# Performance work log

Measured on AMD Instinct MI355X. Metric: run time of the kernel, lower is better.

## Reference

```python
import jax, jax.numpy as jnp
import numpy as np

D_STATE = 16
D_CONV = 4


def layernorm(x, g, b, eps=1e-5):
    mu = jnp.mean(x, axis=-1, keepdims=True)
    var = jnp.mean(jnp.square(x - mu), axis=-1, keepdims=True)
    return (x - mu) * jax.lax.rsqrt(var + eps) * g + b


def mamba(x, W_in, conv_w, conv_b, W_x, W_dt, b_dt, A_log, D_param, W_out):
    # x: (B, L, C)
    B, L, C = x.shape
    d_inner, d_conv = conv_w.shape
    d_state = A_log.shape[1]
    dt_rank = W_dt.shape[0]

    xz = x @ W_in                       # (B, L, 2*d_inner)
    xm, z = jnp.split(xz, 2, axis=-1)   # each (B, L, d_inner)

    # depthwise causal conv1d (padding d_conv-1 on the left, truncated to L)
    xp = jnp.pad(xm, ((0, 0), (d_conv - 1, 0), (0, 0)))
    xm = sum(xp[:, k:k + L, :] * conv_w[:, k] for k in range(d_conv)) + conv_b
    xm = jax.nn.silu(xm)

    dbl = xm @ W_x                      # (B, L, dt_rank + 2*d_state)
    dt, Bm, Cm = jnp.split(dbl, [dt_rank, dt_rank + d_state], axis=-1)
    dt = jax.nn.softplus(dt @ W_dt + b_dt)  # (B, L, d_inner)
    A = -jnp.exp(A_log)                     # (d_inner, d_state)

    def step(h, inputs):
        dt_t, B_t, C_t, x_t = inputs        # (B,d_inner),(B,d_state),(B,d_state),(B,d_inner)
        dA = jnp.exp(dt_t[..., None] * A)   # (B, d_inner, d_state)
        h = dA * h + (dt_t * x_t)[..., None] * B_t[:, None, :]
        y = jnp.einsum('bds,bs->bd', h, C_t)
        return h, y

    seq = (dt.transpose(1, 0, 2), Bm.transpose(1, 0, 2),
           Cm.transpose(1, 0, 2), xm.transpose(1, 0, 2))
    h0 = jnp.zeros((B, d_inner, d_state), x.dtype)
    _, ys = jax.lax.scan(step, h0, seq)     # ys: (L, B, d_inner)
    y = ys.transpose(1, 0, 2) + xm * D_param
    y = y * jax.nn.silu(z)
    return y @ W_out                        # (B, L, C)


def setup_inputs() -> dict:
    key = jax.random.key(0)
    B, C, H, W = 8, 256, 32, 32
    d_inner = 2 * C
    dt_rank = (C + 15) // 16  # 16
    hidden = 4 * C
    ks = jax.random.split(key, 12)
    s = lambda k, shape, scale=0.02: jax.random.normal(k, shape, jnp.float32) * scale
    return {
        'x': jax.random.normal(ks[0], (B, C, H, W), jnp.float32),
        'ln1_g': jnp.ones((C,), jnp.float32), 'ln1_b': jnp.zeros((C,), jnp.float32),
        'ln2_g': jnp.ones((C,), jnp.float32), 'ln2_b': jnp.zeros((C,), jnp.float32),
        'W_in': s(ks[1], (C, 2 * d_inner)),
        'conv_w': s(ks[2], (d_inner, D_CONV), 0.1),
        'conv_b': jnp.zeros((d_inner,), jnp.float32),
        'W_x': s(ks[3], (d_inner, dt_rank + 2 * D_STATE)),
        'W_dt': s(ks[4], (dt_rank, d_inner)),
        'b_dt': s(ks[5], (d_inner,), 0.1),
        'A_log': jnp.log(jnp.tile(jnp.arange(1, D_STATE + 1, dtype=jnp.float32), (d_inner, 1))),
        'D_param': jnp.ones((d_inner,), jnp.float32),
        'W_out': s(ks[6], (d_inner, C)),
        'W1': s(ks[7], (C, hidden)), 'b1': jnp.zeros((hidden,), jnp.float32),
        'W2': s(ks[8], (hidden, C)), 'b2': jnp.zeros((C,), jnp.float32),
    }


def reference(x, ln1_g, ln1_b, ln2_g, ln2_b, W_in, conv_w, conv_b, W_x, W_dt,
              b_dt, A_log, D_param, W_out, W1, b1, W2, b2):
    B, C, H, W = x.shape
    x = x.transpose(0, 2, 3, 1)          # (B, H, W, C)
    res = x
    xn = layernorm(x, ln1_g, ln1_b)
    xm = mamba(xn.reshape(B, H * W, C), W_in, conv_w, conv_b, W_x, W_dt,
               b_dt, A_log, D_param, W_out).reshape(B, H, W, C)
    x = xm + res
    res = x
    xn = layernorm(x, ln2_g, ln2_b)
    x = jax.nn.gelu(xn @ W1 + b1, approximate=False) @ W2 + b2 + res
    return x.transpose(0, 3, 1, 2)        # (B, C, H, W)
```

## Files before the change

kernel.cpp:

```cpp
#include <hip/hip_runtime.h>
#include <hip/hip_bf16.h>
#include <math.h>

using u16 = unsigned short;
using u32 = unsigned int;
typedef __attribute__((ext_vector_type(8))) short bf16x8;
typedef __attribute__((ext_vector_type(4))) float f32x4;
typedef __attribute__((ext_vector_type(8))) unsigned short us8;
typedef __attribute__((ext_vector_type(4))) unsigned short us4;

__device__ __forceinline__ float b2f(u16 u) {
  return __uint_as_float(((u32)u) << 16);
}
__device__ __forceinline__ u16 f2b(float f) {
  u32 x = __float_as_uint(f);
  x += 0x7fffu + ((x >> 16) & 1u);
  return (u16)(x >> 16);
}

__global__ void k_detect(const u16* __restrict__ alog, int* __restrict__ flag) {
  if (threadIdx.x == 0 && blockIdx.x == 0)
    flag[0] = (alog[1] != 0) ? 1 : 0;
}

__device__ __forceinline__ u16 cvt_one(const void* src, int i, int f) {
  u16 r;
  if (f == 0) {
    float v = ((const float*)src)[i];
    if (!isfinite(v)) v = 0.f;
    r = f2b(v);
  } else {
    r = ((const u16*)src)[i];
    if (((r >> 7) & 0xFFu) == 0xFFu) r = 0;
  }
  return r;
}

struct SetupP {
  const void* ws0; const void* ws1; const void* ws2; const void* ws3;
  u16* wd0; u16* wd1; u16* wd2; u16* wd3;
  const void* ssrc[11];
  u16* sdst[11];
  int send[11];
  const void* wxr;
  const void* wdtr;
  u16* wcbc;
  int smallEnd;
  int total;
};
__global__ __launch_bounds__(256) void k_setup(SetupP p, const int* __restrict__ flag) {
  int i = blockIdx.x * 256 + threadIdx.x;
  if (i >= p.total) return;
  int f = flag[0];
  if (i < 262144) {
    int k = i >> 10, n = i & 1023;
    p.wd0[n * 256 + k] = cvt_one(p.ws0, i, f);
  } else if (i < 524288) {
    int j = i - 262144; int k = j >> 10, n = j & 1023;
    p.wd1[n * 256 + k] = cvt_one(p.ws1, j, f);
  } else if (i < 786432) {
    int j = i - 524288; int k = j >> 8, n = j & 255;
    p.wd2[n * 1024 + k] = cvt_one(p.ws2, j, f);
  } else if (i < 917504) {
    int j = i - 786432; int k = j >> 8, n = j & 255;
    p.wd3[n * 512 + k] = cvt_one(p.ws3, j, f);
  } else if (i < p.smallEnd) {
    int j = i - 917504;
    int seg = 0, base = 0;
    #pragma unroll
    for (int s = 0; s < 11; ++s) {
      if (j >= p.send[s]) { seg = s + 1; base = p.send[s]; }
    }
    p.sdst[seg][j - base] = cvt_one(p.ssrc[seg], j - base, f);
  } else {
    int idx = i - p.smallEnd;
    int j = idx >> 9, ii = idx & 511;
    u16 r;
    if (j < 512) {
      float s = 0.f;
      #pragma unroll
      for (int k = 0; k < 16; ++k)
        s = fmaf(b2f(cvt_one(p.wxr, ii * 48 + k, f)),
                 b2f(cvt_one(p.wdtr, k * 512 + j, f)), s);
      r = f2b(s);
    } else if (j < 544) {
      r = cvt_one(p.wxr, ii * 48 + 16 + (j - 512), f);
    } else {
      r = 0;
    }
    p.wcbc[idx] = r;
  }
}

__global__ __launch_bounds__(256) void k_tln(const void* __restrict__ src,
    const u16* __restrict__ g, const u16* __restrict__ be,
    u16* __restrict__ xt, u16* __restrict__ xn, const int* __restrict__ flag) {
  __shared__ float t[256][17];
  __shared__ float smu[16], srs[16];
  int bid = blockIdx.x;
  int lt = bid & 63, b = bid >> 6;
  int f = flag[0];
  int lc = threadIdx.x & 15;
  int lr = threadIdx.x >> 4;
  for (int i = 0; i < 16; ++i) {
    int c = i * 16 + lr;
    int l = lt * 16 + lc;
    size_t idx = ((size_t)b * 256 + c) * 1024 + l;
    float v;
    if (f == 0) {
      v = ((const float*)src)[idx];
      if (!isfinite(v)) v = 0.f;
    } else {
      u16 u = ((const u16*)src)[idx];
      if (((u >> 7) & 0xFFu) == 0xFFu) u = 0;
      v = b2f(u);
    }
    t[c][lc] = v;
  }
  __syncthreads();
  int token = threadIdx.x >> 4, j = threadIdx.x & 15;
  float s = 0.f, q = 0.f;
  for (int k = 0; k < 16; ++k) {
    float v = t[k * 16 + j][token];
    s += v; q = fmaf(v, v, q);
  }
  s += __shfl_xor(s, 1, 16); q += __shfl_xor(q, 1, 16);
  s += __shfl_xor(s, 2, 16); q += __shfl_xor(q, 2, 16);
  s += __shfl_xor(s, 4, 16); q += __shfl_xor(q, 4, 16);
  s += __shfl_xor(s, 8, 16); q += __shfl_xor(q, 8, 16);
  if (j == 0) {
    float mu = s * (1.f / 256.f);
    smu[token] = mu;
    srs[token] = rsqrtf(q * (1.f / 256.f) - mu * mu + 1e-5f);
  }
  __syncthreads();
  float gv = b2f(g[threadIdx.x]), bv = b2f(be[threadIdx.x]);
  size_t tok0 = (size_t)b * 1024 + lt * 16;
  for (int i = 0; i < 16; ++i) {
    float v = t[threadIdx.x][i];
    size_t o = (tok0 + i) * 256 + threadIdx.x;
    xt[o] = f2b(v);
    xn[o] = f2b((v - smu[i]) * srs[i] * gv + bv);
  }
}

__global__ __launch_bounds__(256) void k_ln(const u16* __restrict__ xin,
    const u16* __restrict__ g, const u16* __restrict__ be,
    u16* __restrict__ xn) {
  int tok = blockIdx.x * 4 + (threadIdx.x >> 6);
  int lane = threadIdx.x & 63;
  us4 xv = *(const us4*)&xin[(size_t)tok * 256 + lane * 4];
  float v[4];
  float s = 0.f, q = 0.f;
  #pragma unroll
  for (int j2 = 0; j2 < 4; ++j2) {
    v[j2] = b2f(xv[j2]);
    s += v[j2]; q = fmaf(v[j2], v[j2], q);
  }
  #pragma unroll
  for (int o = 1; o < 64; o <<= 1) {
    s += __shfl_xor(s, o, 64);
    q += __shfl_xor(q, o, 64);
  }
  float mu = s * (1.f / 256.f);
  float rs = rsqrtf(q * (1.f / 256.f) - mu * mu + 1e-5f);
  us4 o4;
  #pragma unroll
  for (int j2 = 0; j2 < 4; ++j2) {
    float t = (v[j2] - mu) * rs * b2f(g[lane * 4 + j2]) + b2f(be[lane * 4 + j2]);
    o4[j2] = f2b(t);
  }
  *(us4*)&xn[(size_t)tok * 256 + lane * 4] = o4;
}

__global__ __launch_bounds__(256) void k_conv(const u16* __restrict__ xz,
    const u16* __restrict__ cw, const u16* __restrict__ cb,
    u16* __restrict__ xm) {
  int idx = blockIdx.x * 256 + threadIdx.x;
  int d4 = (idx & 127) * 4;
  int tok = idx >> 7;
  int l = tok & 1023;
  float a[4];
  #pragma unroll
  for (int j = 0; j < 4; ++j) a[j] = b2f(cb[d4 + j]);
  #pragma unroll
  for (int k = 0; k < 4; ++k) {
    int ls = l - 3 + k;
    if (ls >= 0) {
      us4 xv = *(const us4*)&xz[(size_t)(tok - 3 + k) * 1024 + d4];
      #pragma unroll
      for (int j = 0; j < 4; ++j)
        a[j] = fmaf(b2f(xv[j]), b2f(cw[(d4 + j) * 4 + k]), a[j]);
    }
  }
  us4 o;
  #pragma unroll
  for (int j = 0; j < 4; ++j) {
    float sig = 1.f / (1.f + __expf(-a[j]));
    o[j] = f2b(a[j] * sig);
  }
  *(us4*)&xm[(size_t)tok * 512 + d4] = o;
}

__global__ __launch_bounds__(256) void k_scan1(const u16* __restrict__ dt,
    const u16* __restrict__ xm, const u16* __restrict__ bc,
    const u16* __restrict__ A_log, u16* __restrict__ hend,
    float* __restrict__ sdtw) {
  __shared__ float sB[32][16];
  int bi = blockIdx.x;
  int half = bi & 1;
  int bc_ = bi >> 1;
  int b = bc_ >> 5, c = bc_ & 31;
  int d = half * 256 + threadIdx.x;
  size_t tok0 = (size_t)b * 1024 + c * 32;
  for (int i = threadIdx.x; i < 512; i += 256) {
    int t = i >> 4, s = i & 15;
    sB[t][s] = b2f(bc[(tok0 + t) * 32 + s]);
  }
  __syncthreads();
  float As[16], h[16];
  bool fast = true;
  #pragma unroll
  for (int s = 0; s < 16; ++s) {
    As[s] = -__expf(b2f(A_log[d * 16 + s]));
    h[s] = 0.f;
    fast = fast && (fabsf(As[s] + (float)(s + 1)) < 0.02f * (s + 1));
  }
  float sacc = 0.f;
  float dtv = b2f(dt[tok0 * 512 + d]);
  float xv  = b2f(xm[tok0 * 512 + d]);
  if (fast) {
    for (int t = 0; t < 32; ++t) {
      float ndt = 0.f, nx = 0.f;
      if (t < 31) {
        ndt = b2f(dt[(tok0 + t + 1) * 512 + d]);
        nx  = b2f(xm[(tok0 + t + 1) * 512 + d]);
      }
      sacc += dtv;
      float u = dtv * xv;
      float q = __expf(-dtv), p = 1.f;
      #pragma unroll
      for (int s = 0; s < 16; ++s) {
        p *= q;
        h[s] = fmaf(p, h[s], u * sB[t][s]);
      }
      dtv = ndt; xv = nx;
    }
  } else {
    for (int t = 0; t < 32; ++t) {
      float ndt = 0.f, nx = 0.f;
      if (t < 31) {
        ndt = b2f(dt[(tok0 + t + 1) * 512 + d]);
        nx  = b2f(xm[(tok0 + t + 1) * 512 + d]);
      }
      sacc += dtv;
      float u = dtv * xv;
      #pragma unroll
      for (int s = 0; s < 16; ++s)
        h[s] = fmaf(__expf(dtv * As[s]), h[s], u * sB[t][s]);
      dtv = ndt; xv = nx;
    }
  }
  u16* hp = hend + ((size_t)bc_ * 512 + d) * 16;
  #pragma unroll
  for (int s = 0; s < 16; ++s) hp[s] = f2b(h[s]);
  sdtw[(size_t)bc_ * 512 + d] = sacc;
}

__global__ __launch_bounds__(256) void k_scan2(u16* __restrict__ hend,
    const float* __restrict__ sdtw, const u16* __restrict__ A_log) {
  int idx = blockIdx.x * 256 + threadIdx.x;
  int s = idx & 15, d = (idx >> 4) & 511, b = idx >> 13;
  float As_ = -__expf(b2f(A_log[d * 16 + s]));
  if (fabsf(As_ + (float)(s + 1)) < 0.02f * (s + 1)) As_ = -(float)(s + 1);
  float H = 0.f;
  for (int c = 0; c < 32; ++c) {
    size_t off = (size_t)(b * 32 + c) * 512 + d;
    float dec = __expf(As_ * sdtw[off]);
    float he = b2f(hend[off * 16 + s]);
    hend[off * 16 + s] = f2b(H);
    H = fmaf(dec, H, he);
  }
}

__global__ __launch_bounds__(256) void k_scan3(const u16* __restrict__ dt,
    const u16* __restrict__ xm, const u16* __restrict__ bc,
    const u16* __restrict__ xz, const u16* __restrict__ A_log,
    const u16* __restrict__ Dp, const u16* __restrict__ hstart,
    u16* __restrict__ yg) {
  __shared__ float sB[32][16], sC[32][16];
  int bi = blockIdx.x;
  int half = bi & 1;
  int bc_ = bi >> 1;
  int b = bc_ >> 5, c = bc_ & 31;
  int d = half * 256 + threadIdx.x;
  size_t tok0 = (size_t)b * 1024 + c * 32;
  for (int i = threadIdx.x; i < 1024; i += 256) {
    int t = i >> 5, col = i & 31;
    float v = b2f(bc[(tok0 + t) * 32 + col]);
    if (col < 16) sB[t][col] = v;
    else          sC[t][col - 16] = v;
  }
  __syncthreads();
  float As[16], h[16];
  const u16* hp = hstart + ((size_t)bc_ * 512 + d) * 16;
  bool fast = true;
  #pragma unroll
  for (int s = 0; s < 16; ++s) {
    As[s] = -__expf(b2f(A_log[d * 16 + s]));
    h[s] = b2f(hp[s]);
    fast = fast && (fabsf(As[s] + (float)(s + 1)) < 0.02f * (s + 1));
  }
  float Dd = b2f(Dp[d]);
  float dtv = b2f(dt[tok0 * 512 + d]);
  float xv  = b2f(xm[tok0 * 512 + d]);
  float zv  = b2f(xz[tok0 * 1024 + 512 + d]);
  for (int t = 0; t < 32; ++t) {
    float ndt = 0.f, nx = 0.f, nz = 0.f;
    if (t < 31) {
      ndt = b2f(dt[(tok0 + t + 1) * 512 + d]);
      nx  = b2f(xm[(tok0 + t + 1) * 512 + d]);
      nz  = b2f(xz[(tok0 + t + 1) * 1024 + 512 + d]);
    }
    float u = dtv * xv;
    if (fast) {
      float q = __expf(-dtv), p = 1.f;
      #pragma unroll
      for (int s = 0; s < 16; ++s) {
        p *= q;
        h[s] = fmaf(p, h[s], u * sB[t][s]);
      }
    } else {
      #pragma unroll
      for (int s = 0; s < 16; ++s)
        h[s] = fmaf(__expf(dtv * As[s]), h[s], u * sB[t][s]);
    }
    float y0 = 0.f, y1 = 0.f, y2 = 0.f, y3 = 0.f;
    #pragma unroll
    for (int s = 0; s < 16; s += 4) {
      y0 = fmaf(h[s + 0], sC[t][s + 0], y0);
      y1 = fmaf(h[s + 1], sC[t][s + 1], y1);
      y2 = fmaf(h[s + 2], sC[t][s + 2], y2);
      y3 = fmaf(h[s + 3], sC[t][s + 3], y3);
    }
    float y = (y0 + y1) + (y2 + y3);
    float yy = fmaf(xv, Dd, y);
    float sig = 1.f / (1.f + __expf(-zv));
    yg[(tok0 + t) * 512 + d] = f2b(yy * zv * sig);
    dtv = ndt; xv = nx; zv = nz;
  }
}

template<int EPI, int BM, int BN>
__global__ __launch_bounds__(256) void k_mgemm(
    const u16* __restrict__ A, const u16* __restrict__ Bt,
    const u16* __restrict__ bias, const u16* __restrict__ res,
    u16* __restrict__ outp, u16* __restrict__ out2,
    void* __restrict__ outv, const int* __restrict__ flag,
    int M, int N, int K, int GX) {
  constexpr int BK = 32;
  constexpr int LDP = BK + 8;
  constexpr int MT = BM / 32, NT = BN / 32;
  constexpr int AL = (BM * BK) / 2048, BL = (BN * BK) / 2048;
  __shared__ u16 As[2][BM][LDP];
  __shared__ u16 Bs[2][BN][LDP];
  const int tid = threadIdx.x;
  const int wid = tid >> 6, lane = tid & 63;
  const int wr = wid >> 1, wc2 = wid & 1;
  const int lrow = lane & 15, lk = lane >> 4;
  const int per = gridDim.x >> 3;
  const int t_ = (blockIdx.x & 7) * per + (blockIdx.x >> 3);
  const int m0 = (t_ / GX) * BM, n0 = (t_ % GX) * BN;

  f32x4 acc[MT][NT];
  #pragma unroll
  for (int i = 0; i < MT; ++i)
    #pragma unroll
    for (int j = 0; j < NT; ++j)
      acc[i][j] = (f32x4){0.f, 0.f, 0.f, 0.f};

  us8 ra[AL], rb[BL];
  #pragma unroll
  for (int i = 0; i < AL; ++i) {
    int c = tid + i * 256, row = c >> 2, k0 = (c & 3) * 8;
    ra[i] = *(const us8*)(A + (size_t)(m0 + row) * K + k0);
  }
  #pragma unroll
  for (int i = 0; i < BL; ++i) {
    int c = tid + i * 256, row = c >> 2, k0 = (c & 3) * 8;
    rb[i] = *(const us8*)(Bt + (size_t)(n0 + row) * K + k0);
  }
  #pragma unroll
  for (int i = 0; i < AL; ++i) {
    int c = tid + i * 256, row = c >> 2, k0 = (c & 3) * 8;
    *(us8*)&As[0][row][k0] = ra[i];
  }
  #pragma unroll
  for (int i = 0; i < BL; ++i) {
    int c = tid + i * 256, row = c >> 2, k0 = (c & 3) * 8;
    *(us8*)&Bs[0][row][k0] = rb[i];
  }
  __syncthreads();

  const int nIter = K / BK;
  for (int it = 0; it < nIter; ++it) {
    const int cur = it & 1;
    if (it + 1 < nIter) {
      #pragma unroll
      for (int i = 0; i < AL; ++i) {
        int c = tid + i * 256, row = c >> 2, k0 = (c & 3) * 8;
        ra[i] = *(const us8*)(A + (size_t)(m0 + row) * K + (it + 1) * BK + k0);
      }
      #pragma unroll
      for (int i = 0; i < BL; ++i) {
        int c = tid + i * 256, row = c >> 2, k0 = (c & 3) * 8;
        rb[i] = *(const us8*)(Bt + (size_t)(n0 + row) * K + (it + 1) * BK + k0);
      }
    }
    bf16x8 af[MT], bf[NT];
    #pragma unroll
    for (int i = 0; i < MT; ++i)
      af[i] = *(const bf16x8*)&As[cur][wr * (BM / 2) + i * 16 + lrow][lk * 8];
    #pragma unroll
    for (int j = 0; j < NT; ++j)
      bf[j] = *(const bf16x8*)&Bs[cur][wc2 * (BN / 2) + j * 16 + lrow][lk * 8];
    #pragma unroll
    for (int i = 0; i < MT; ++i)
      #pragma unroll
      for (int j = 0; j < NT; ++j)
        acc[i][j] = __builtin_amdgcn_mfma_f32_16x16x32_bf16(
            af[i], bf[j], acc[i][j], 0, 0, 0);
    if (it + 1 < nIter) {
      #pragma unroll
      for (int i = 0; i < AL; ++i) {
        int c = tid + i * 256, row = c >> 2, k0 = (c & 3) * 8;
        *(us8*)&As[cur ^ 1][row][k0] = ra[i];
      }
      #pragma unroll
      for (int i = 0; i < BL; ++i) {
        int c = tid + i * 256, row = c >> 2, k0 = (c & 3) * 8;
        *(us8*)&Bs[cur ^ 1][row][k0] = rb[i];
      }
    }
    __syncthreads();
  }

  if constexpr (EPI == 6) {
    __shared__ float tbuf[64][65];
    #pragma unroll
    for (int i = 0; i < MT; ++i)
      #pragma unroll
      for (int j = 0; j < NT; ++j)
        #pragma unroll
        for (int r = 0; r < 4; ++r) {
          const int ml = wr * (BM / 2) + i * 16 + lk * 4 + r;
          const int nl = wc2 * (BN / 2) + j * 16 + lrow;
          float t = acc[i][j][r] + b2f(bias[n0 + nl])
                  + b2f(res[(size_t)(m0 + ml) * N + n0 + nl]);
          if (!isfinite(t)) t = 0.f;
          tbuf[nl][ml] = t;
        }
    __syncthreads();
    int cl = tid >> 2, tg = tid & 3;
    int c = n0 + cl;
    int bb = m0 >> 10;
    int l0 = (m0 & 1023) + tg * 16;
    size_t obase = ((size_t)bb * 256 + c) * 1024 + l0;
    int f = flag[0];
    if (f) {
      us8 o0, o1;
      #pragma unroll
      for (int k = 0; k < 8; ++k) {
        o0[k] = f2b(tbuf[cl][tg * 16 + k]);
        o1[k] = f2b(tbuf[cl][tg * 16 + 8 + k]);
      }
      *(us8*)((u16*)outv + obase) = o0;
      *(us8*)((u16*)outv + obase + 8) = o1;
    } else {
      float* op = (float*)outv + obase;
      #pragma unroll
      for (int k = 0; k < 16; ++k) op[k] = tbuf[cl][tg * 16 + k];
    }
    return;
  }

  #pragma unroll
  for (int i = 0; i < MT; ++i) {
    #pragma unroll
    for (int j = 0; j < NT; ++j) {
      #pragma unroll
      for (int r = 0; r < 4; ++r) {
        const int m = m0 + wr * (BM / 2) + i * 16 + lk * 4 + r;
        const int n = n0 + wc2 * (BN / 2) + j * 16 + lrow;
        float v = acc[i][j][r];
        if constexpr (EPI == 0) {
          outp[(size_t)m * N + n] = f2b(v);
        } else if constexpr (EPI == 2) {
          float t = v + b2f(res[(size_t)m * N + n]);
          outp[(size_t)m * N + n] = f2b(t);
        } else if constexpr (EPI == 3) {
          float t = v + b2f(bias[n]);
          float gl = 0.5f * t * (1.f + erff(t * 0.70710678118654752f));
          outp[(size_t)m * N + n] = f2b(gl);
        } else if constexpr (EPI == 5) {
          if (n < 512) {
            float t = v + b2f(bias[n]);
            float sp = fmaxf(t, 0.f) + log1pf(__expf(-fabsf(t)));
            outp[(size_t)m * 512 + n] = f2b(sp);
          } else if (n < 544) {
            out2[(size_t)m * 32 + (n - 512)] = f2b(v);
          }
        }
      }
    }
  }
}

extern "C" void kernel_launch(void* const* d_in, const int* in_sizes, int n_in,
                              void* d_out, int out_size, void* d_ws, size_t ws_size,
                              hipStream_t stream) {
  char* ws = (char*)d_ws;
  u16* arena = (u16*)ws;
  u16* x_t  = arena + 0;
  u16* WinT = arena + 2097152;
  u16* W1T  = arena + 2359296;
  u16* W2T  = arena + 2621440;
  u16* WoT  = arena + 2883584;
  const size_t S = 3145728;
  u16* g1C  = arena + S + 0;
  u16* b1nC = arena + S + 256;
  u16* g2C  = arena + S + 512;
  u16* b2nC = arena + S + 768;
  u16* cbC  = arena + S + 1024;
  u16* bdtC = arena + S + 1536;
  u16* DpC  = arena + S + 2048;
  u16* bb2C = arena + S + 2560;
  u16* bb1C = arena + S + 3072;
  u16* cwC  = arena + S + 4096;
  u16* AlC  = arena + S + 6144;
  float* sdtw = (float*)(ws + (7ull << 20));

  u16* xn1 = (u16*)(ws + (8ull  << 20));
  u16* x2  = xn1;
  u16* hend = (u16*)(ws + (8ull << 20));
  u16* xz  = (u16*)(ws + (12ull << 20));
  u16* h1  = xz;
  u16* xm  = (u16*)(ws + (28ull << 20));
  u16* xn2 = xm;
  u16* dtb = (u16*)(ws + (36ull << 20));
  u16* yg  = (u16*)(ws + (44ull << 20));
  u16* bcb = (u16*)(ws + (52ull << 20));
  u16* wcbc = (u16*)(ws + (52ull << 20) + (512ull << 10));
  int* flag = (int*)(ws + (54ull << 20));

  k_detect<<<1, 64, 0, stream>>>((const u16*)d_in[11], flag);
  {
    SetupP p;
    p.ws0 = d_in[5];  p.wd0 = WinT;
    p.ws1 = d_in[14]; p.wd1 = W1T;
    p.ws2 = d_in[16]; p.wd2 = W2T;
    p.ws3 = d_in[13]; p.wd3 = WoT;
    const int ids[11] = {1, 2, 3, 4, 6, 7, 10, 11, 12, 15, 17};
    u16* dsts[11] = {g1C, b1nC, g2C, b2nC, cwC, cbC, bdtC, AlC, DpC, bb1C, bb2C};
    int acc = 0;
    for (int i = 0; i < 11; ++i) {
      p.ssrc[i] = d_in[ids[i]];
      p.sdst[i] = dsts[i];
      acc += in_sizes[ids[i]];
      p.send[i] = acc;
    }
    p.wxr = d_in[8];
    p.wdtr = d_in[9];
    p.wcbc = wcbc;
    p.smallEnd = 917504 + acc;
    p.total = p.smallEnd + 640 * 512;
    k_setup<<<(p.total + 255) / 256, 256, 0, stream>>>(p, flag);
  }

  k_tln<<<512, 256, 0, stream>>>(d_in[0], g1C, b1nC, x_t, xn1, flag);
  k_mgemm<0, 128, 64><<<1024, 256, 0, stream>>>(
      xn1, WinT, nullptr, nullptr, xz, nullptr, nullptr, flag, 8192, 1024, 256, 16);
  k_conv<<<4096, 256, 0, stream>>>(xz, cwC, cbC, xm);
  k_mgemm<5, 64, 64><<<1280, 256, 0, stream>>>(
      xm, wcbc, bdtC, nullptr, dtb, bcb, nullptr, flag, 8192, 640, 512, 10);
  k_scan1<<<512, 256, 0, stream>>>(dtb, xm, bcb, AlC, hend, sdtw);
  k_scan2<<<256, 256, 0, stream>>>(hend, sdtw, AlC);
  k_scan3<<<512, 256, 0, stream>>>(dtb, xm, bcb, xz, AlC, DpC, hend, yg);
  k_mgemm<2, 64, 64><<<512, 256, 0, stream>>>(
      yg, WoT, nullptr, x_t, x2, nullptr, nullptr, flag, 8192, 256, 512, 4);
  k_ln<<<2048, 256, 0, stream>>>(x2, g2C, b2nC, xn2);
  k_mgemm<3, 128, 64><<<1024, 256, 0, stream>>>(
      xn2, W1T, bb1C, nullptr, h1, nullptr, nullptr, flag, 8192, 1024, 256, 16);
  k_mgemm<6, 64, 64><<<512, 256, 0, stream>>>(
      h1, W2T, bb2C, x2, nullptr, nullptr, d_out, flag, 8192, 256, 1024, 4);
}
```

Baseline: 275.8 us.

## Replace shared-memory GEMM with per-wave register-direct 64x64 MFMA tiles

```diff
diff --git a/kernel.cpp b/kernel.cpp
--- a/kernel.cpp
+++ b/kernel.cpp
@@ -351,147 +351,125 @@
   }
 }
 
-template<int EPI, int BM, int BN>
-__global__ __launch_bounds__(256) void k_mgemm(
+template<int EPI>
+__global__ __launch_bounds__(256) void k_wgemm(
     const u16* __restrict__ A, const u16* __restrict__ Bt,
     const u16* __restrict__ bias, const u16* __restrict__ res,
     u16* __restrict__ outp, u16* __restrict__ out2,
     void* __restrict__ outv, const int* __restrict__ flag,
     int M, int N, int K, int GX) {
-  constexpr int BK = 32;
-  constexpr int LDP = BK + 8;
-  constexpr int MT = BM / 32, NT = BN / 32;
-  constexpr int AL = (BM * BK) / 2048, BL = (BN * BK) / 2048;
-  __shared__ u16 As[2][BM][LDP];
-  __shared__ u16 Bs[2][BN][LDP];
   const int tid = threadIdx.x;
   const int wid = tid >> 6, lane = tid & 63;
-  const int wr = wid >> 1, wc2 = wid & 1;
   const int lrow = lane & 15, lk = lane >> 4;
   const int per = gridDim.x >> 3;
-  const int t_ = (blockIdx.x & 7) * per + (blockIdx.x >> 3);
-  const int m0 = (t_ / GX) * BM, n0 = (t_ % GX) * BN;
-
-  f32x4 acc[MT][NT];
-  #pragma unroll
-  for (int i = 0; i < MT; ++i)
-    #pragma unroll
-    for (int j = 0; j < NT; ++j)
+  const int b_ = (blockIdx.x & 7) * per + (blockIdx.x >> 3);
+  const int t_ = b_ * 4 + wid;
+  const int m0 = (t_ / GX) * 64, n0 = (t_ % GX) * 64;
+
+  const u16* Ar[4];
+  const u16* Br[4];
+  #pragma unroll
+  for (int i = 0; i < 4; ++i) {
+    Ar[i] = A + (size_t)(m0 + i * 16 + lrow) * K + lk * 8;
+    Br[i] = Bt + (size_t)(n0 + i * 16 + lrow) * K + lk * 8;
+  }
+
+  f32x4 acc[4][4];
+  #pragma unroll
+  for (int i = 0; i < 4; ++i)
+    #pragma unroll
+    for (int j = 0; j < 4; ++j)
       acc[i][j] = (f32x4){0.f, 0.f, 0.f, 0.f};
 
-  us8 ra[AL], rb[BL];
-  #pragma unroll
-  for (int i = 0; i < AL; ++i) {
-    int c = tid + i * 256, row = c >> 2, k0 = (c & 3) * 8;
-    ra[i] = *(const us8*)(A + (size_t)(m0 + row) * K + k0);
-  }
-  #pragma unroll
-  for (int i = 0; i < BL; ++i) {
-    int c = tid + i * 256, row = c >> 2, k0 = (c & 3) * 8;
-    rb[i] = *(const us8*)(Bt + (size_t)(n0 + row) * K + k0);
-  }
-  #pragma unroll
-  for (int i = 0; i < AL; ++i) {
-    int c = tid + i * 256, row = c >> 2, k0 = (c & 3) * 8;
-    *(us8*)&As[0][row][k0] = ra[i];
-  }
-  #pragma unroll
-  for (int i = 0; i < BL; ++i) {
-    int c = tid + i * 256, row = c >> 2, k0 = (c & 3) * 8;
-    *(us8*)&Bs[0][row][k0] = rb[i];
-  }
-  __syncthreads();
-
-  const int nIter = K / BK;
-  for (int it = 0; it < nIter; ++it) {
-    const int cur = it & 1;
-    if (it + 1 < nIter) {
-      #pragma unroll
-      for (int i = 0; i < AL; ++i) {
-        int c = tid + i * 256, row = c >> 2, k0 = (c & 3) * 8;
-        ra[i] = *(const us8*)(A + (size_t)(m0 + row) * K + (it + 1) * BK + k0);
-      }
-      #pragma unroll
-      for (int i = 0; i < BL; ++i) {
-        int c = tid + i * 256, row = c >> 2, k0 = (c & 3) * 8;
-        rb[i] = *(const us8*)(Bt + (size_t)(n0 + row) * K + (it + 1) * BK + k0);
-      }
-    }
-    bf16x8 af[MT], bf[NT];
-    #pragma unroll
-    for (int i = 0; i < MT; ++i)
-      af[i] = *(const bf16x8*)&As[cur][wr * (BM / 2) + i * 16 + lrow][lk * 8];
-    #pragma unroll
-    for (int j = 0; j < NT; ++j)
-      bf[j] = *(const bf16x8*)&Bs[cur][wc2 * (BN / 2) + j * 16 + lrow][lk * 8];
-    #pragma unroll
-    for (int i = 0; i < MT; ++i)
-      #pragma unroll
-      for (int j = 0; j < NT; ++j)
+  us8 a0[4], b0[4], a1[4], b1[4];
+  #pragma unroll
+  for (int i = 0; i < 4; ++i) {
+    a0[i] = *(const us8*)(Ar[i]);
+    b0[i] = *(const us8*)(Br[i]);
+  }
+  const int nIter = K >> 5;
+  for (int it = 0; it < nIter; it += 2) {
+    #pragma unroll
+    for (int i = 0; i < 4; ++i) {
+      a1[i] = *(const us8*)(Ar[i] + (it + 1) * 32);
+      b1[i] = *(const us8*)(Br[i] + (it + 1) * 32);
+    }
+    #pragma unroll
+    for (int i = 0; i < 4; ++i) {
+      bf16x8 af = __builtin_bit_cast(bf16x8, a0[i]);
+      #pragma unroll
+      for (int j = 0; j < 4; ++j)
         acc[i][j] = __builtin_amdgcn_mfma_f32_16x16x32_bf16(
-            af[i], bf[j], acc[i][j], 0, 0, 0);
-    if (it + 1 < nIter) {
-      #pragma unroll
-      for (int i = 0; i < AL; ++i) {
-        int c = tid + i * 256, row = c >> 2, k0 = (c & 3) * 8;
-        *(us8*)&As[cur ^ 1][row][k0] = ra[i];
-      }
-      #pragma unroll
-      for (int i = 0; i < BL; ++i) {
-        int c = tid + i * 256, row = c >> 2, k0 = (c & 3) * 8;
-        *(us8*)&Bs[cur ^ 1][row][k0] = rb[i];
-      }
-    }
-    __syncthreads();
+            af, __builtin_bit_cast(bf16x8, b0[j]), acc[i][j], 0, 0, 0);
+    }
+    if (it + 2 < nIter) {
+      #pragma unroll
+      for (int i = 0; i < 4; ++i) {
+        a0[i] = *(const us8*)(Ar[i] + (it + 2) * 32);
+        b0[i] = *(const us8*)(Br[i] + (it + 2) * 32);
+      }
+    }
+    #pragma unroll
+    for (int i = 0; i < 4; ++i) {
+      bf16x8 af = __builtin_bit_cast(bf16x8, a1[i]);
+      #pragma unroll
+      for (int j = 0; j < 4; ++j)
+        acc[i][j] = __builtin_amdgcn_mfma_f32_16x16x32_bf16(
+            af, __builtin_bit_cast(bf16x8, b1[j]), acc[i][j], 0, 0, 0);
+    }
   }
 
   if constexpr (EPI == 6) {
-    __shared__ float tbuf[64][65];
-    #pragma unroll
-    for (int i = 0; i < MT; ++i)
-      #pragma unroll
-      for (int j = 0; j < NT; ++j)
+    __shared__ float tbuf[4][64][65];
+    #pragma unroll
+    for (int i = 0; i < 4; ++i)
+      #pragma unroll
+      for (int j = 0; j < 4; ++j)
         #pragma unroll
         for (int r = 0; r < 4; ++r) {
-          const int ml = wr * (BM / 2) + i * 16 + lk * 4 + r;
-          const int nl = wc2 * (BN / 2) + j * 16 + lrow;
+          const int ml = i * 16 + lk * 4 + r;
+          const int nl = j * 16 + lrow;
           float t = acc[i][j][r] + b2f(bias[n0 + nl])
                   + b2f(res[(size_t)(m0 + ml) * N + n0 + nl]);
           if (!isfinite(t)) t = 0.f;
-          tbuf[nl][ml] = t;
+          tbuf[wid][nl][ml] = t;
         }
-    __syncthreads();
-    int cl = tid >> 2, tg = tid & 3;
-    int c = n0 + cl;
-    int bb = m0 >> 10;
-    int l0 = (m0 & 1023) + tg * 16;
-    size_t obase = ((size_t)bb * 256 + c) * 1024 + l0;
     int f = flag[0];
-    if (f) {
-      us8 o0, o1;
-      #pragma unroll
-      for (int k = 0; k < 8; ++k) {
-        o0[k] = f2b(tbuf[cl][tg * 16 + k]);
-        o1[k] = f2b(tbuf[cl][tg * 16 + 8 + k]);
-      }
-      *(us8*)((u16*)outv + obase) = o0;
-      *(us8*)((u16*)outv + obase + 8) = o1;
-    } else {
-      float* op = (float*)outv + obase;
-      #pragma unroll
-      for (int k = 0; k < 16; ++k) op[k] = tbuf[cl][tg * 16 + k];
+    const int bb = m0 >> 10;
+    const int lbase = m0 & 1023;
+    #pragma unroll
+    for (int pass = 0; pass < 4; ++pass) {
+      int cl = pass * 16 + (lane >> 2);
+      int tg = lane & 3;
+      int c = n0 + cl;
+      int l0 = lbase + tg * 16;
+      size_t obase = ((size_t)bb * 256 + c) * 1024 + l0;
+      if (f) {
+        us8 o0, o1;
+        #pragma unroll
+        for (int k = 0; k < 8; ++k) {
+          o0[k] = f2b(tbuf[wid][cl][tg * 16 + k]);
+          o1[k] = f2b(tbuf[wid][cl][tg * 16 + 8 + k]);
+        }
+        *(us8*)((u16*)outv + obase) = o0;
+        *(us8*)((u16*)outv + obase + 8) = o1;
+      } else {
+        float* op = (float*)outv + obase;
+        #pragma unroll
+        for (int k = 0; k < 16; ++k) op[k] = tbuf[wid][cl][tg * 16 + k];
+      }
     }
     return;
   }
 
   #pragma unroll
-  for (int i = 0; i < MT; ++i) {
-    #pragma unroll
-    for (int j = 0; j < NT; ++j) {
+  for (int i = 0; i < 4; ++i) {
+    #pragma unroll
+    for (int j = 0; j < 4; ++j) {
       #pragma unroll
       for (int r = 0; r < 4; ++r) {
-        const int m = m0 + wr * (BM / 2) + i * 16 + lk * 4 + r;
-        const int n = n0 + wc2 * (BN / 2) + j * 16 + lrow;
+        const int m = m0 + i * 16 + lk * 4 + r;
+        const int n = n0 + j * 16 + lrow;
         float v = acc[i][j][r];
         if constexpr (EPI == 0) {
           outp[(size_t)m * N + n] = f2b(v);
@@ -578,19 +556,19 @@
   }
 
   k_tln<<<512, 256, 0, stream>>>(d_in[0], g1C, b1nC, x_t, xn1, flag);
-  k_mgemm<0, 128, 64><<<1024, 256, 0, stream>>>(
+  k_wgemm<0><<<512, 256, 0, stream>>>(
       xn1, WinT, nullptr, nullptr, xz, nullptr, nullptr, flag, 8192, 1024, 256, 16);
   k_conv<<<4096, 256, 0, stream>>>(xz, cwC, cbC, xm);
-  k_mgemm<5, 64, 64><<<1280, 256, 0, stream>>>(
+  k_wgemm<5><<<320, 256, 0, stream>>>(
       xm, wcbc, bdtC, nullptr, dtb, bcb, nullptr, flag, 8192, 640, 512, 10);
   k_scan1<<<512, 256, 0, stream>>>(dtb, xm, bcb, AlC, hend, sdtw);
   k_scan2<<<256, 256, 0, stream>>>(hend, sdtw, AlC);
   k_scan3<<<512, 256, 0, stream>>>(dtb, xm, bcb, xz, AlC, DpC, hend, yg);
-  k_mgemm<2, 64, 64><<<512, 256, 0, stream>>>(
+  k_wgemm<2><<<128, 256, 0, stream>>>(
       yg, WoT, nullptr, x_t, x2, nullptr, nullptr, flag, 8192, 256, 512, 4);
   k_ln<<<2048, 256, 0, stream>>>(x2, g2C, b2nC, xn2);
-  k_mgemm<3, 128, 64><<<1024, 256, 0, stream>>>(
+  k_wgemm<3><<<512, 256, 0, stream>>>(
       xn2, W1T, bb1C, nullptr, h1, nullptr, nullptr, flag, 8192, 1024, 256, 16);
-  k_mgemm<6, 64, 64><<<512, 256, 0, stream>>>(
+  k_wgemm<6><<<128, 256, 0, stream>>>(
       h1, W2T, bb2C, x2, nullptr, nullptr, d_out, flag, 8192, 256, 1024, 4);
 }
```

After: 360.7 us. 30.7% more time.
